# Kernel optimization log

Measured on AMD Instinct MI355X. Metric: run time of the kernel, lower is better.

Reference implementation:

```python
import jax
import jax.numpy as jnp
import numpy as np

B = 128          # graphs per batch
N = 1024         # nodes per graph
EG = 16384       # edges per graph (shared structure, repeated edge_weight)
F_IN = 64        # num_features
HID = 128        # hid_channels (ChebConv out)
K = 3            # Chebyshev order
C1 = HID // 2    # conv1d out channels
C2 = C1 // 2     # fc1 out
N_CLASSES = 4
POWER_ITERS = 50


def setup_inputs() -> dict:
    key = jax.random.key(0)
    ks = jax.random.split(key, 8)
    x = jax.random.normal(ks[0], (B * N, F_IN), dtype=jnp.float32)
    edge_index = jax.random.randint(ks[1], (2, EG), 0, N, dtype=jnp.int32)
    edge_weight = jax.random.uniform(ks[2], (EG,), dtype=jnp.float32)
    cheb_W = 0.05 * jax.random.normal(ks[3], (K, F_IN, HID), dtype=jnp.float32)
    cheb_b = jnp.zeros((HID,), jnp.float32)
    conv1d_W = 0.05 * jax.random.normal(ks[4], (C1, HID), dtype=jnp.float32)
    conv1d_b = jnp.zeros((C1,), jnp.float32)
    fc1_W = 0.01 * jax.random.normal(ks[5], (C2, C1 * N), dtype=jnp.float32)
    fc1_b = jnp.zeros((C2,), jnp.float32)
    fc2_W = 0.05 * jax.random.normal(ks[6], (N_CLASSES, C2), dtype=jnp.float32)
    fc2_b = jnp.zeros((N_CLASSES,), jnp.float32)
    return {"x": x, "edge_index": edge_index, "edge_weight": edge_weight,
            "cheb_W": cheb_W, "cheb_b": cheb_b,
            "conv1d_W": conv1d_W, "conv1d_b": conv1d_b,
            "fc1_W": fc1_W, "fc1_b": fc1_b, "fc2_W": fc2_W, "fc2_b": fc2_b}


def _lambda_max(edge_index, w):
    # LaplacianLambdaMax(normalization=None): largest eig of L = D - W, on raw
    # (un-relu'd) edge_attr, computed as a non-differentiable data transform.
    src, dst = edge_index[0], edge_index[1]
    deg = jax.ops.segment_sum(w, src, num_segments=N)

    def mv(v):  # L @ v
        return deg * v - jax.ops.segment_sum(w * v[src], dst, num_segments=N)

    def body(i, v):
        u = mv(v)
        return u / (jnp.linalg.norm(u) + 1e-12)

    v0 = jnp.ones((N,), jnp.float32) / np.float32(np.sqrt(N))
    v = jax.lax.fori_loop(0, POWER_ITERS, body, v0)
    return jax.lax.stop_gradient(jnp.vdot(v, mv(v)))


def _forward(x, edge_index, edge_weight, cheb_W, cheb_b, conv1d_W, conv1d_b,
             fc1_W, fc1_b, fc2_W, fc2_b):
    lmax = _lambda_max(edge_index, edge_weight)

    # Tile the shared per-graph edge structure over the batch (block-diagonal).
    offs = jnp.arange(B, dtype=jnp.int32) * N                  # [B]
    src = (edge_index[0][None, :] + offs[:, None]).reshape(-1)  # [B*EG]
    dst = (edge_index[1][None, :] + offs[:, None]).reshape(-1)  # [B*EG]
    w = jax.nn.relu(jnp.tile(edge_weight, B))                   # relu(edge_attr)

    BN = B * N
    deg = jax.ops.segment_sum(w, src, num_segments=BN)          # [BN]
    scale = 2.0 / lmax

    def lhat_mv(X):  # (2 L / lmax - I) @ X ; L = D - W
        agg = jax.ops.segment_sum(w[:, None] * X[src], dst, num_segments=BN)
        return scale * (deg[:, None] * X - agg) - X

    # Chebyshev recursion, K = 3
    tx0 = x                               # [BN, F_IN]
    tx1 = lhat_mv(tx0)
    tx2 = 2.0 * lhat_mv(tx1) - tx0
    h = tx0 @ cheb_W[0] + tx1 @ cheb_W[1] + tx2 @ cheb_W[2] + cheb_b  # [BN, HID]

    # 1x1 conv1d over the node axis + relu
    hb = h.reshape(B, N, HID)
    c = jax.nn.relu(jnp.einsum('bnh,ch->bcn', hb, conv1d_W)
                    + conv1d_b[None, :, None])                  # [B, C1, N]
    flat = c.reshape(B, C1 * N)

    z = flat @ fc1_W.T + fc1_b
    z = z @ fc2_W.T + fc2_b                                     # [B, N_CLASSES]
    return jax.nn.softmax(z, axis=1)


def reference(x, edge_index, edge_weight, cheb_W, cheb_b, conv1d_W, conv1d_b,
              fc1_W, fc1_b, fc2_W, fc2_b):
    return _forward(x, edge_index, edge_weight, cheb_W, cheb_b, conv1d_W,
                    conv1d_b, fc1_W, fc1_b, fc2_W, fc2_b)
```

## Files before the change

### kernel.cpp

```cpp
#include <hip/hip_runtime.h>
#include <math.h>

#define BATCH 128
#define NNODE 1024
#define EG 16384
#define F_IN 64
#define HID 128
#define C1 64
#define C2 32
#define NCLS 4
#define POWER_ITERS 50
#define BN (BATCH * NNODE)
#define RMAX 28
#define NORM_EVERY 5

typedef float f32x4 __attribute__((ext_vector_type(4)));
typedef __bf16 bf16x8 __attribute__((ext_vector_type(8)));
typedef unsigned short u16x4 __attribute__((ext_vector_type(4)));

__device__ inline unsigned short f2bf(float f) {
    unsigned int u = __float_as_uint(f);
    u += 0x7fffu + ((u >> 16) & 1u);
    return (unsigned short)(u >> 16);
}
__device__ inline float bf2f(unsigned short h) {
    return __uint_as_float((unsigned int)h << 16);
}

__global__ __launch_bounds__(1024) void k_csr(
    const int* __restrict__ ei, const float* __restrict__ ew,
    int* __restrict__ ptr_g, float* __restrict__ dgr_g,
    float* __restrict__ dgl_g, int2* __restrict__ packed,
    int2* __restrict__ packed2)
{
    __shared__ int   cnt[NNODE];
    __shared__ float dgr[NNODE];
    __shared__ float dgl[NNODE];
    __shared__ int   s[NNODE];
    __shared__ int   base[NNODE];
    const int t = threadIdx.x;

    cnt[t] = 0; dgr[t] = 0.f; dgl[t] = 0.f;

    int es[16], ed[16];
    float w[16];
#pragma unroll
    for (int i = 0; i < 16; ++i) {
        const int e = i * 1024 + t;
        es[i] = ei[e];
        ed[i] = ei[EG + e];
        w[i]  = ew[e];
    }
    __syncthreads();
#pragma unroll
    for (int i = 0; i < 16; ++i) {
        atomicAdd(&cnt[ed[i]], 1);
        atomicAdd(&dgr[es[i]], w[i]);
        atomicAdd(&dgl[es[i]], fmaxf(w[i], 0.f));
    }
    __syncthreads();
    dgr_g[t] = dgr[t];
    dgl_g[t] = dgl[t];

    const int v = cnt[t];
    s[t] = v;
    __syncthreads();
    for (int o = 1; o < 1024; o <<= 1) {
        const int add = (t >= o) ? s[t - o] : 0;
        __syncthreads();
        s[t] += add;
        __syncthreads();
    }
    const int excl = s[t] - v;
    ptr_g[t] = excl;
    base[t]  = excl;
    if (t == 1023) ptr_g[1024] = s[1023];
    __syncthreads();

#pragma unroll
    for (int i = 0; i < 16; ++i) {
        const int p = atomicAdd(&base[ed[i]], 1);
        packed[p]  = make_int2(__float_as_int(w[i]), es[i]);
        packed2[p] = make_int2(__float_as_int(fmaxf(w[i], 0.f)), es[i] << 8);
    }
}

__global__ __launch_bounds__(256) void k_cvtw(
    const float* __restrict__ chebW, const float* __restrict__ convW,
    const float* __restrict__ scal,
    unsigned short* __restrict__ wcatT, unsigned short* __restrict__ cvw)
{
    const int i = blockIdx.x * 256 + threadIdx.x;
    const float s = scal[1];
    if (i < 24576) {
        const int n = i / 192, kk = i % 192;
        const int k = kk & 63;
        const float w0 = chebW[k * 128 + n];
        const float w1 = chebW[8192 + k * 128 + n];
        const float w2 = chebW[16384 + k * 128 + n];
        float val;
        if (kk < 64)       val = w0 - w1 + w2;
        else if (kk < 128) val = s * (w1 - 4.f * w2);
        else               val = 2.f * s * s * w2;
        wcatT[i] = f2bf(val);
    }
    const int j = i - 24576;
    if (j >= 0 && j < 8192) cvw[j] = f2bf(convW[j]);
}

__global__ __launch_bounds__(1024) void k_fused(
    const float* __restrict__ in,
    const int2* __restrict__ pk_raw, const int2* __restrict__ pk2,
    const int* __restrict__ ptrg,
    const float* __restrict__ dgr, const float* __restrict__ dgl,
    float* __restrict__ vstate, float* __restrict__ scal,
    float* __restrict__ out32, unsigned short* __restrict__ tcat,
    int slice, int writeX, int it0, int it1, int finalize)
{
    __shared__ float vA[NNODE];
    __shared__ float vB[NNODE];
    __shared__ float red[17];
    const int t = threadIdx.x;

    if (blockIdx.x == 0) {
        const int p0 = ptrg[t], p1 = ptrg[t + 1];
        float w[RMAX];
        int src[RMAX];
#pragma unroll
        for (int i = 0; i < RMAX; ++i) {
            if (p0 + i < p1) {
                const int2 e = pk_raw[p0 + i];
                w[i] = __int_as_float(e.x);
                src[i] = e.y;
            } else {
                w[i] = 0.f;
                src[i] = 0;
            }
        }
        const int tp0 = p0 + RMAX;
        const float dgv = dgr[t];

        vA[t] = (it0 == 0) ? 0.03125f : vstate[t];
        __syncthreads();

        float* cur = vA;
        float* nxt = vB;

        for (int it = it0; it < it1; ++it) {
            float u = dgv * cur[t];
#pragma unroll
            for (int i = 0; i < RMAX; ++i) u -= w[i] * cur[src[i]];
            for (int p = tp0; p < p1; ++p) {
                const int2 e = pk_raw[p];
                u -= __int_as_float(e.x) * cur[e.y];
            }
            if ((it % NORM_EVERY) == NORM_EVERY - 1) {
                float sr = u * u;
#pragma unroll
                for (int o = 32; o > 0; o >>= 1) sr += __shfl_down(sr, o, 64);
                if ((t & 63) == 0) red[t >> 6] = sr;
                __syncthreads();
                if (t < 64) {
                    float xs = (t < 16) ? red[t] : 0.f;
#pragma unroll
                    for (int o = 8; o > 0; o >>= 1) xs += __shfl_down(xs, o, 64);
                    if (t == 0) red[16] = 1.0f / (sqrtf(xs) + 1e-12f);
                }
                __syncthreads();
                nxt[t] = u * red[16];
            } else {
                nxt[t] = u;
            }
            __syncthreads();
            float* tmp = cur; cur = nxt; nxt = tmp;
        }

        if (!finalize) {
            vstate[t] = cur[t];
            return;
        }
        float u = dgv * cur[t];
#pragma unroll
        for (int i = 0; i < RMAX; ++i) u -= w[i] * cur[src[i]];
        for (int p = tp0; p < p1; ++p) {
            const int2 e = pk_raw[p];
            u -= __int_as_float(e.x) * cur[e.y];
        }
        float sr = cur[t] * u;
#pragma unroll
        for (int o = 32; o > 0; o >>= 1) sr += __shfl_down(sr, o, 64);
        if ((t & 63) == 0) red[t >> 6] = sr;
        __syncthreads();
        if (t == 0) {
            float lm = 0.f;
            for (int i = 0; i < 16; ++i) lm += red[i];
            scal[0] = lm;
            scal[1] = 2.0f / lm;
        }
        return;
    }

    const int b1   = blockIdx.x - 1;
    const int bid  = ((b1 & 7) << 10) + (b1 >> 3);
    const int lane = threadIdx.x & 63;
    const int gnode = __builtin_amdgcn_readfirstlane(bid * 16 + (threadIdx.x >> 6));
    const int b = gnode >> 10, d = gnode & 1023;

    const int p0 = __builtin_amdgcn_readfirstlane(ptrg[d]);
    const int p1 = __builtin_amdgcn_readfirstlane(ptrg[d + 1]);
    const char* xb = (const char*)(in + (size_t)b * (NNODE * F_IN));

    float acc = 0.f;
    int p = p0;
    for (; p + 4 <= p1; p += 4) {
        const int2 e0 = pk2[p],     e1 = pk2[p + 1];
        const int2 e2 = pk2[p + 2], e3 = pk2[p + 3];
        const float v0 = ((const float*)(xb + (unsigned)e0.y))[lane];
        const float v1 = ((const float*)(xb + (unsigned)e1.y))[lane];
        const float v2 = ((const float*)(xb + (unsigned)e2.y))[lane];
        const float v3 = ((const float*)(xb + (unsigned)e3.y))[lane];
        acc += __int_as_float(e0.x) * v0;
        acc += __int_as_float(e1.x) * v1;
        acc += __int_as_float(e2.x) * v2;
        acc += __int_as_float(e3.x) * v3;
    }
    for (; p < p1; ++p) {
        const int2 e = pk2[p];
        acc += __int_as_float(e.x) * ((const float*)(xb + (unsigned)e.y))[lane];
    }

    const size_t gi = (size_t)gnode * F_IN + lane;
    const float xv = in[gi];
    const float o = dgl[d] * xv - acc;
    if (out32) out32[gi] = o;
    tcat[(size_t)gnode * 192 + slice * 64 + lane] = f2bf(o);
    if (writeX) tcat[(size_t)gnode * 192 + lane] = f2bf(xv);
}

__global__ __launch_bounds__(256) void k_cheb_mfma(
    const unsigned short* __restrict__ tcat,
    const unsigned short* __restrict__ wcatT,
    const unsigned short* __restrict__ cvw,
    const float* __restrict__ chebB, const float* __restrict__ convB,
    unsigned short* __restrict__ cout)
{
    __shared__ __align__(16) char smem[49152];
    __shared__ float cb_s[HID];
    __shared__ float cvb_s[C1];

    const int t    = threadIdx.x;
    const int lane = t & 63;
    const int wid  = t >> 6;
    const int l15  = lane & 15;
    const int l4   = lane >> 4;
    const int rbase = blockIdx.x * 128;
    const int bb = rbase >> 10;
    const int n0 = rbase & 1023;

    if (t < HID) cb_s[t] = chebB[t];
    if (t < C1)  cvb_s[t] = convB[t];

    for (int it = 0; it < 12; ++it) {
        const int gslot = it * 256 + t;
        const int n = gslot / 24, q = gslot % 24;
        const bf16x8 v = *(const bf16x8*)(wcatT + n * 192 + q * 8);
        *(bf16x8*)(smem + n * 384 + ((q ^ (n & 7)) << 4)) = v;
    }
    __syncthreads();

    const int rw = rbase + wid * 32;
    f32x4 acc[2][8];
#pragma unroll
    for (int m = 0; m < 2; ++m)
#pragma unroll
        for (int n = 0; n < 8; ++n) acc[m][n] = (f32x4)(0.f);

    const unsigned short* ta = tcat + (size_t)(rw + l15) * 192 + l4 * 8;
    bf16x8 a0 = *(const bf16x8*)(ta);
    bf16x8 a1 = *(const bf16x8*)(ta + 16 * 192);

#pragma unroll
    for (int ks = 0; ks < 6; ++ks) {
        bf16x8 na0, na1;
        if (ks < 5) {
            na0 = *(const bf16x8*)(ta + (ks + 1) * 32);
            na1 = *(const bf16x8*)(ta + 16 * 192 + (ks + 1) * 32);
        }
        const int kb = ks * 4 + l4;
#pragma unroll
        for (int nb = 0; nb < 8; ++nb) {
            const int n = nb * 16 + l15;
            const bf16x8 bv =
                *(const bf16x8*)(smem + n * 384 + ((kb ^ (n & 7)) << 4));
            acc[0][nb] = __builtin_amdgcn_mfma_f32_16x16x32_bf16(
                a0, bv, acc[0][nb], 0, 0, 0);
            acc[1][nb] = __builtin_amdgcn_mfma_f32_16x16x32_bf16(
                a1, bv, acc[1][nb], 0, 0, 0);
        }
        a0 = na0; a1 = na1;
    }
    __syncthreads();

#pragma unroll
    for (int mf = 0; mf < 2; ++mf)
#pragma unroll
        for (int nb = 0; nb < 8; ++nb) {
            const int c = nb * 16 + l15;
            const int slot = c >> 3;
            const float cb = cb_s[c];
#pragma unroll
            for (int reg = 0; reg < 4; ++reg) {
                const int node = wid * 32 + mf * 16 + l4 * 4 + reg;
                *(unsigned short*)(smem + node * 256 +
                                   ((slot ^ (node & 7)) << 4) + (c & 7) * 2) =
                    f2bf(acc[mf][nb][reg] + cb);
            }
        }
    for (int it = 0; it < 4; ++it) {
        const int gslot = it * 256 + t;
        const int c1i = gslot >> 4, q = gslot & 15;
        const bf16x8 v = *(const bf16x8*)(cvw + c1i * 128 + q * 8);
// ... 46 lines not shown
        const int j = i >> 8, k = i & 255;
        Wt[k * 33 + j] = W[(size_t)j * (C1 * NNODE) + k0 + k];
    }
    __syncthreads();

    const int j = t & 31, bg = t >> 5;
    float acc[16];
#pragma unroll
    for (int i = 0; i < 16; ++i) acc[i] = 0.f;

    const unsigned short* cb = cf + (size_t)(bg * 16) * (C1 * NNODE) + k0;
    for (int k4 = 0; k4 < 64; ++k4) {
        const int kb = k4 * 4;
        const float w0 = Wt[(kb + 0) * 33 + j];
        const float w1 = Wt[(kb + 1) * 33 + j];
        const float w2 = Wt[(kb + 2) * 33 + j];
        const float w3 = Wt[(kb + 3) * 33 + j];
#pragma unroll
        for (int i = 0; i < 16; ++i) {
            const u16x4 cv = *(const u16x4*)&cb[(size_t)i * (C1 * NNODE) + kb];
            acc[i] += bf2f(cv[0]) * w0 + bf2f(cv[1]) * w1 +
                      bf2f(cv[2]) * w2 + bf2f(cv[3]) * w3;
        }
    }
#pragma unroll
    for (int i = 0; i < 16; ++i)
        part[(size_t)g * 4096 + (size_t)(bg * 16 + i) * 32 + j] = acc[i];
}

__global__ __launch_bounds__(256) void k_red(
    const float* __restrict__ part, float* __restrict__ z)
{
    const int o = blockIdx.x * 256 + threadIdx.x;
    float s = 0.f;
    for (int g = 0; g < 256; ++g) s += part[(size_t)g * 4096 + o];
    z[o] = s;
}

__global__ __launch_bounds__(128) void k_head(
    const float* __restrict__ z, const float* __restrict__ b1,
    const float* __restrict__ W2, const float* __restrict__ b2,
    float* __restrict__ outp)
{
    const int b = threadIdx.x;
    float a[32];
#pragma unroll
    for (int j = 0; j < 32; ++j) a[j] = z[b * 32 + j] + b1[j];
    float l[4];
#pragma unroll
    for (int c = 0; c < 4; ++c) {
        float s = b2[c];
#pragma unroll
        for (int j = 0; j < 32; ++j) s += W2[c * 32 + j] * a[j];
        l[c] = s;
    }
    const float m = fmaxf(fmaxf(l[0], l[1]), fmaxf(l[2], l[3]));
    const float e0 = expf(l[0] - m), e1 = expf(l[1] - m);
    const float e2 = expf(l[2] - m), e3 = expf(l[3] - m);
    const float inv = 1.f / (e0 + e1 + e2 + e3);
    outp[b * 4 + 0] = e0 * inv;
    outp[b * 4 + 1] = e1 * inv;
    outp[b * 4 + 2] = e2 * inv;
    outp[b * 4 + 3] = e3 * inv;
}

extern "C" void kernel_launch(void* const* d_in, const int* in_sizes, int n_in,
                              void* d_out, int out_size, void* d_ws, size_t ws_size,
                              hipStream_t stream)
{
    const float* x     = (const float*)d_in[0];
    const int*   ei    = (const int*)d_in[1];
    const float* ew    = (const float*)d_in[2];
    const float* chebW = (const float*)d_in[3];
    const float* chebB = (const float*)d_in[4];
    const float* convW = (const float*)d_in[5];
    const float* convB = (const float*)d_in[6];
    const float* fc1W  = (const float*)d_in[7];
    const float* fc1B  = (const float*)d_in[8];
    const float* fc2W  = (const float*)d_in[9];
    const float* fc2B  = (const float*)d_in[10];
    float* out = (float*)d_out;

    char* ws = (char*)d_ws;
    float* scal   = (float*)(ws + 0);
    float* vstate = (float*)(ws + 4096);
    char*  partb = ws + 8192;
    int*   ptr  = (int*)(partb + 8192);
    float* dgr  = (float*)(partb + 16384);
    float* dgl  = (float*)(partb + 20480);
    int2*  pk   = (int2*)(partb + 24576);
    unsigned short* wcatT = (unsigned short*)(partb + 262144);
    unsigned short* cvwB  = (unsigned short*)(partb + 327680);
    int2*  pk2  = (int2*)(partb + 458752);
    float* part = (float*)partb;
    float* z    = (float*)(ws + 8192 + 4194304);
    float* y1   = (float*)(ws + 8192 + 4194304 + 65536);
    unsigned short* tcat = (unsigned short*)((char*)y1 + 33554432);
    unsigned short* cbuf = (unsigned short*)((char*)tcat + 50331648);

    k_csr <<<dim3(1), dim3(1024), 0, stream>>>(ei, ew, ptr, dgr, dgl, pk, pk2);

    k_fused<<<dim3(BN / 16 + 1), dim3(1024), 0, stream>>>(
        x, pk, pk2, ptr, dgr, dgl, vstate, scal,
        y1, tcat, 1, 1, 0, 25, 0);
    k_fused<<<dim3(BN / 16 + 1), dim3(1024), 0, stream>>>(
        y1, pk, pk2, ptr, dgr, dgl, vstate, scal,
        (float*)nullptr, tcat, 2, 0, 25, 50, 1);

    k_cvtw<<<dim3(128), dim3(256), 0, stream>>>(chebW, convW, scal, wcatT, cvwB);

    k_cheb_mfma<<<dim3(BN / 128), dim3(256), 0, stream>>>(
        tcat, wcatT, cvwB, chebB, convB, cbuf);

    k_fc1<<<dim3(256), dim3(256), 0, stream>>>(cbuf, fc1W, part);
    k_red<<<dim3(16), dim3(256), 0, stream>>>(part, z);
    k_head<<<dim3(1), dim3(128), 0, stream>>>(z, fc1B, fc2W, fc2B, out);
}
```

Measured before the change: 268.0 us.

## Fuse both graph propagation hops into one LDS-resident kernel per graph slice

The two propagation launches, which went through a global fp32 intermediate, are replaced by one kernel. Each block holds a 16-feature slice of one graph's node features in shared memory (128 KB) and runs both Laplacian hops from LDS. The power iteration now runs all 50 steps in block 0 of that single launch. The edge list is padded to multiples of four per node so four edges are gathered in parallel per wavefront and combined with shuffles. This removes the y1 round trip, one launch, and the scattered global gathers, at the cost of only 513 large blocks with low occupancy and 4x redundant edge traversal per graph.

```diff
diff --git a/kernel.cpp b/kernel.cpp
--- a/kernel.cpp
+++ b/kernel.cpp
@@ -29,15 +29,17 @@
 
 __global__ __launch_bounds__(1024) void k_csr(
     const int* __restrict__ ei, const float* __restrict__ ew,
-    int* __restrict__ ptr_g, float* __restrict__ dgr_g,
-    float* __restrict__ dgl_g, int2* __restrict__ packed,
-    int2* __restrict__ packed2)
+    int* __restrict__ ptr_g, int* __restrict__ ptr2_g,
+    float* __restrict__ dgr_g, float* __restrict__ dgl_g,
+    int2* __restrict__ packed, int2* __restrict__ packed2)
 {
     __shared__ int   cnt[NNODE];
     __shared__ float dgr[NNODE];
     __shared__ float dgl[NNODE];
     __shared__ int   s[NNODE];
+    __shared__ int   s2[NNODE];
     __shared__ int   base[NNODE];
+    __shared__ int   base2[NNODE];
     const int t = threadIdx.x;
 
     cnt[t] = 0; dgr[t] = 0.f; dgl[t] = 0.f;
@@ -62,27 +64,33 @@
     dgr_g[t] = dgr[t];
     dgl_g[t] = dgl[t];
 
-    const int v = cnt[t];
-    s[t] = v;
+    const int v  = cnt[t];
+    const int v4 = (v + 3) & ~3;
+    s[t] = v; s2[t] = v4;
     __syncthreads();
     for (int o = 1; o < 1024; o <<= 1) {
-        const int add = (t >= o) ? s[t - o] : 0;
+        const int a  = (t >= o) ? s[t - o]  : 0;
+        const int a2 = (t >= o) ? s2[t - o] : 0;
         __syncthreads();
-        s[t] += add;
+        s[t] += a; s2[t] += a2;
         __syncthreads();
     }
-    const int excl = s[t] - v;
-    ptr_g[t] = excl;
-    base[t]  = excl;
-    if (t == 1023) ptr_g[1024] = s[1023];
+    const int excl  = s[t]  - v;
+    const int excl2 = s2[t] - v4;
+    ptr_g[t]  = excl;  base[t]  = excl;
+    ptr2_g[t] = excl2; base2[t] = excl2;
+    if (t == 1023) { ptr_g[1024] = s[1023]; ptr2_g[1024] = s2[1023]; }
     __syncthreads();
 
 #pragma unroll
     for (int i = 0; i < 16; ++i) {
-        const int p = atomicAdd(&base[ed[i]], 1);
-        packed[p]  = make_int2(__float_as_int(w[i]), es[i]);
-        packed2[p] = make_int2(__float_as_int(fmaxf(w[i], 0.f)), es[i] << 8);
-    }
+        const int p  = atomicAdd(&base[ed[i]],  1);
+        const int p2 = atomicAdd(&base2[ed[i]], 1);
+        packed[p]   = make_int2(__float_as_int(w[i]), es[i]);
+        packed2[p2] = make_int2(__float_as_int(fmaxf(w[i], 0.f)), es[i] << 6);
+    }
+    for (int j = excl2 + v; j < excl2 + v4; ++j)
+        packed2[j] = make_int2(0, 0);
 }
 
 __global__ __launch_bounds__(256) void k_cvtw(
@@ -108,21 +116,20 @@
     if (j >= 0 && j < 8192) cvw[j] = f2bf(convW[j]);
 }
 
-__global__ __launch_bounds__(1024) void k_fused(
-    const float* __restrict__ in,
+__global__ __launch_bounds__(1024) void k_prop2(
+    const float* __restrict__ x,
     const int2* __restrict__ pk_raw, const int2* __restrict__ pk2,
-    const int* __restrict__ ptrg,
+    const int* __restrict__ ptrg, const int* __restrict__ ptr2g,
     const float* __restrict__ dgr, const float* __restrict__ dgl,
-    float* __restrict__ vstate, float* __restrict__ scal,
-    float* __restrict__ out32, unsigned short* __restrict__ tcat,
-    int slice, int writeX, int it0, int it1, int finalize)
-{
-    __shared__ float vA[NNODE];
-    __shared__ float vB[NNODE];
-    __shared__ float red[17];
+    float* __restrict__ scal, unsigned short* __restrict__ tcat)
+{
+    __shared__ float smem[32768];
     const int t = threadIdx.x;
 
     if (blockIdx.x == 0) {
+        float* vA  = smem;
+        float* vB  = smem + 1024;
+        float* red = smem + 2048;
         const int p0 = ptrg[t], p1 = ptrg[t + 1];
         float w[RMAX];
         int src[RMAX];
@@ -140,13 +147,13 @@
         const int tp0 = p0 + RMAX;
         const float dgv = dgr[t];
 
-        vA[t] = (it0 == 0) ? 0.03125f : vstate[t];
+        vA[t] = 0.03125f;
         __syncthreads();
 
         float* cur = vA;
         float* nxt = vB;
 
-        for (int it = it0; it < it1; ++it) {
+        for (int it = 0; it < POWER_ITERS; ++it) {
             float u = dgv * cur[t];
 #pragma unroll
             for (int i = 0; i < RMAX; ++i) u -= w[i] * cur[src[i]];
@@ -161,10 +168,10 @@
                 if ((t & 63) == 0) red[t >> 6] = sr;
                 __syncthreads();
                 if (t < 64) {
-                    float xs = (t < 16) ? red[t] : 0.f;
-#pragma unroll
-                    for (int o = 8; o > 0; o >>= 1) xs += __shfl_down(xs, o, 64);
-                    if (t == 0) red[16] = 1.0f / (sqrtf(xs) + 1e-12f);
+                    float xs2 = (t < 16) ? red[t] : 0.f;
+#pragma unroll
+                    for (int o = 8; o > 0; o >>= 1) xs2 += __shfl_down(xs2, o, 64);
+                    if (t == 0) red[16] = 1.0f / (sqrtf(xs2) + 1e-12f);
                 }
                 __syncthreads();
                 nxt[t] = u * red[16];
@@ -175,10 +182,6 @@
             float* tmp = cur; cur = nxt; nxt = tmp;
         }
 
-        if (!finalize) {
-            vstate[t] = cur[t];
-            return;
-        }
         float u = dgv * cur[t];
 #pragma unroll
         for (int i = 0; i < RMAX; ++i) u -= w[i] * cur[src[i]];
@@ -200,41 +203,51 @@
         return;
     }
 
-    const int b1   = blockIdx.x - 1;
-    const int bid  = ((b1 & 7) << 10) + (b1 >> 3);
-    const int lane = threadIdx.x & 63;
-    const int gnode = __builtin_amdgcn_readfirstlane(bid * 16 + (threadIdx.x >> 6));
-    const int b = gnode >> 10, d = gnode & 1023;
-
-    const int p0 = __builtin_amdgcn_readfirstlane(ptrg[d]);
-    const int p1 = __builtin_amdgcn_readfirstlane(ptrg[d + 1]);
-    const char* xb = (const char*)(in + (size_t)b * (NNODE * F_IN));
-
-    float acc = 0.f;
-    int p = p0;
-    for (; p + 4 <= p1; p += 4) {
-        const int2 e0 = pk2[p],     e1 = pk2[p + 1];
-        const int2 e2 = pk2[p + 2], e3 = pk2[p + 3];
-        const float v0 = ((const float*)(xb + (unsigned)e0.y))[lane];
-        const float v1 = ((const float*)(xb + (unsigned)e1.y))[lane];
-        const float v2 = ((const float*)(xb + (unsigned)e2.y))[lane];
-        const float v3 = ((const float*)(xb + (unsigned)e3.y))[lane];
-        acc += __int_as_float(e0.x) * v0;
-        acc += __int_as_float(e1.x) * v1;
-        acc += __int_as_float(e2.x) * v2;
-        acc += __int_as_float(e3.x) * v3;
-    }
-    for (; p < p1; ++p) {
-        const int2 e = pk2[p];
-        acc += __int_as_float(e.x) * ((const float*)(xb + (unsigned)e.y))[lane];
-    }
-
-    const size_t gi = (size_t)gnode * F_IN + lane;
-    const float xv = in[gi];
-    const float o = dgl[d] * xv - acc;
-    if (out32) out32[gi] = o;
-    tcat[(size_t)gnode * 192 + slice * 64 + lane] = f2bf(o);
-    if (writeX) tcat[(size_t)gnode * 192 + lane] = f2bf(xv);
+    const int bb = blockIdx.x - 1;
+    const int g  = bb >> 2;
+    const int c  = bb & 3;
+    float* xs = smem;
+    float* ys = smem + 16384;
+
+    const float* xg = x + (size_t)g * (NNODE * F_IN) + c * 16;
+    unsigned short* tg = tcat + (size_t)g * NNODE * 192 + c * 16;
+
+    for (int i = t; i < 16384; i += 1024) {
+        const int n = i >> 4, f = i & 15;
+        const float xv = xg[n * 64 + f];
+        xs[i] = xv;
+        tg[n * 192 + f] = f2bf(xv);
+    }
+    __syncthreads();
+
+    const int wv   = t >> 6;
+    const int lane = t & 63;
+    const int slot = lane >> 4;
+    const int f    = lane & 15;
+
+    for (int pass = 0; pass < 2; ++pass) {
+        const float* srcv = pass ? ys : xs;
+        for (int d = wv; d < NNODE; d += 16) {
+            const int q0 = __builtin_amdgcn_readfirstlane(ptr2g[d]);
+            const int q1 = __builtin_amdgcn_readfirstlane(ptr2g[d + 1]);
+            float acc = 0.f;
+            for (int p = q0; p < q1; p += 4) {
+                const int2 e = pk2[p + slot];
+                const float vv =
+                    *(const float*)((const char*)srcv + e.y + (f << 2));
+                acc += __int_as_float(e.x) * vv;
+            }
+            acc += __shfl_xor(acc, 16, 64);
+            acc += __shfl_xor(acc, 32, 64);
+            const float xv = srcv[d * 16 + f];
+            const float y = dgl[d] * xv - acc;
+            if (lane < 16) {
+                if (pass == 0) ys[d * 16 + f] = y;
+                tg[d * 192 + (pass + 1) * 64 + f] = f2bf(y);
+            }
+        }
+        __syncthreads();
+    }
 }
 
 __global__ __launch_bounds__(256) void k_cheb_mfma(
@@ -449,30 +462,26 @@
     float* out = (float*)d_out;
 
     char* ws = (char*)d_ws;
-    float* scal   = (float*)(ws + 0);
-    float* vstate = (float*)(ws + 4096);
+    float* scal = (float*)(ws + 0);
     char*  partb = ws + 8192;
-    int*   ptr  = (int*)(partb + 8192);
-    float* dgr  = (float*)(partb + 16384);
-    float* dgl  = (float*)(partb + 20480);
-    int2*  pk   = (int2*)(partb + 24576);
-    unsigned short* wcatT = (unsigned short*)(partb + 262144);
-    unsigned short* cvwB  = (unsigned short*)(partb + 327680);
-    int2*  pk2  = (int2*)(partb + 458752);
+    int*   ptr   = (int*)(partb + 8192);
+    int*   ptr2  = (int*)(partb + 16384);
+    float* dgr   = (float*)(partb + 24576);
+    float* dgl   = (float*)(partb + 28672);
+    int2*  pk    = (int2*)(partb + 32768);
+    int2*  pk2   = (int2*)(partb + 163840);
+    unsigned short* wcatT = (unsigned short*)(partb + 327680);
+    unsigned short* cvwB  = (unsigned short*)(partb + 393216);
     float* part = (float*)partb;
     float* z    = (float*)(ws + 8192 + 4194304);
-    float* y1   = (float*)(ws + 8192 + 4194304 + 65536);
-    unsigned short* tcat = (unsigned short*)((char*)y1 + 33554432);
+    unsigned short* tcat = (unsigned short*)(ws + 8192 + 4194304 + 65536);
     unsigned short* cbuf = (unsigned short*)((char*)tcat + 50331648);
 
-    k_csr <<<dim3(1), dim3(1024), 0, stream>>>(ei, ew, ptr, dgr, dgl, pk, pk2);
-
-    k_fused<<<dim3(BN / 16 + 1), dim3(1024), 0, stream>>>(
-        x, pk, pk2, ptr, dgr, dgl, vstate, scal,
-        y1, tcat, 1, 1, 0, 25, 0);
-    k_fused<<<dim3(BN / 16 + 1), dim3(1024), 0, stream>>>(
-        y1, pk, pk2, ptr, dgr, dgl, vstate, scal,
-        (float*)nullptr, tcat, 2, 0, 25, 50, 1);
+    k_csr<<<dim3(1), dim3(1024), 0, stream>>>(ei, ew, ptr, ptr2, dgr, dgl,
+                                              pk, pk2);
+
+    k_prop2<<<dim3(513), dim3(1024), 0, stream>>>(
+        x, pk, pk2, ptr, ptr2, dgr, dgl, scal, tcat);
 
     k_cvtw<<<dim3(128), dim3(256), 0, stream>>>(chebW, convW, scal, wcatT, cvwB);
 
```

Result: slower. 520.6 us (+94.2%).

## Replace sparse graph aggregation with dense bf16 adjacency MFMA GEMM

Applied to the files above, without the earlier changes.

Builds a dense 1024x1024 adjacency matrix of relu'd edge weights, stores it in bf16, and runs both Chebyshev aggregation passes as dense MFMA matrix multiplies against per-graph transposed bf16 feature tiles staged in LDS. This replaces the per-edge gather loops, which are latency-bound. New kernels zero the matrix, convert it to bf16, and transpose x. The dense product does far more arithmetic than the sparse one (about 16 edges per row against 1024 columns), and the second-pass input y1 is now rounded to bf16, so precision drops.

```diff
diff --git a/kernel.cpp b/kernel.cpp
--- a/kernel.cpp
+++ b/kernel.cpp
@@ -17,6 +17,7 @@
 typedef float f32x4 __attribute__((ext_vector_type(4)));
 typedef __bf16 bf16x8 __attribute__((ext_vector_type(8)));
 typedef unsigned short u16x4 __attribute__((ext_vector_type(4)));
+typedef unsigned short u16x8 __attribute__((ext_vector_type(8)));
 
 __device__ inline unsigned short f2bf(float f) {
     unsigned int u = __float_as_uint(f);
@@ -27,11 +28,16 @@
     return __uint_as_float((unsigned int)h << 16);
 }
 
+__global__ __launch_bounds__(1024) void k_zm(float* __restrict__ M32)
+{
+    M32[(size_t)blockIdx.x * 1024 + threadIdx.x] = 0.f;
+}
+
 __global__ __launch_bounds__(1024) void k_csr(
     const int* __restrict__ ei, const float* __restrict__ ew,
     int* __restrict__ ptr_g, float* __restrict__ dgr_g,
     float* __restrict__ dgl_g, int2* __restrict__ packed,
-    int2* __restrict__ packed2)
+    float* __restrict__ M32)
 {
     __shared__ int   cnt[NNODE];
     __shared__ float dgr[NNODE];
@@ -57,6 +63,7 @@
         atomicAdd(&cnt[ed[i]], 1);
         atomicAdd(&dgr[es[i]], w[i]);
         atomicAdd(&dgl[es[i]], fmaxf(w[i], 0.f));
+        atomicAdd(&M32[(size_t)ed[i] * 1024 + es[i]], fmaxf(w[i], 0.f));
     }
     __syncthreads();
     dgr_g[t] = dgr[t];
@@ -66,9 +73,9 @@
     s[t] = v;
     __syncthreads();
     for (int o = 1; o < 1024; o <<= 1) {
-        const int add = (t >= o) ? s[t - o] : 0;
+        const int a = (t >= o) ? s[t - o] : 0;
         __syncthreads();
-        s[t] += add;
+        s[t] += a;
         __syncthreads();
     }
     const int excl = s[t] - v;
@@ -80,8 +87,237 @@
 #pragma unroll
     for (int i = 0; i < 16; ++i) {
         const int p = atomicAdd(&base[ed[i]], 1);
-        packed[p]  = make_int2(__float_as_int(w[i]), es[i]);
-        packed2[p] = make_int2(__float_as_int(fmaxf(w[i], 0.f)), es[i] << 8);
+        packed[p] = make_int2(__float_as_int(w[i]), es[i]);
+    }
+}
+
+__global__ __launch_bounds__(256) void k_cvt_m(
+    const float* __restrict__ M32, unsigned short* __restrict__ M16)
+{
+    const int i = blockIdx.x * 256 + threadIdx.x;
+    const f32x4 v = ((const f32x4*)M32)[i];
+    u16x4 o;
+    o[0] = f2bf(v[0]); o[1] = f2bf(v[1]); o[2] = f2bf(v[2]); o[3] = f2bf(v[3]);
+    *(u16x4*)(M16 + (size_t)i * 4) = o;
+}
+
+__global__ __launch_bounds__(256) void k_xpose(
+    const float* __restrict__ x, unsigned short* __restrict__ xB,
+    unsigned short* __restrict__ tcat)
+{
+    __shared__ unsigned short tile[64 * 66];
+    const int t = threadIdx.x;
+    const int g = blockIdx.x >> 4;
+    const int sp = blockIdx.x & 15;
+    const int n0 = sp * 64;
+
+    const float* xg = x + (size_t)g * (NNODE * F_IN);
+#pragma unroll
+    for (int it = 0; it < 4; ++it) {
+        const int nl = it * 16 + (t >> 4);
+        const int f  = (t & 15) * 4;
+        const f32x4 v = *(const f32x4*)(xg + (size_t)(n0 + nl) * 64 + f);
+        u16x4 o;
+        o[0] = f2bf(v[0]); o[1] = f2bf(v[1]); o[2] = f2bf(v[2]); o[3] = f2bf(v[3]);
+        *(u16x4*)(tcat + ((size_t)(g * 1024 + n0 + nl)) * 192 + f) = o;
+#pragma unroll
+        for (int j = 0; j < 4; ++j) tile[(f + j) * 66 + nl] = o[j];
+    }
+    __syncthreads();
+
+    unsigned short* xg2 = xB + (size_t)g * 65536;
+#pragma unroll
+    for (int it = 0; it < 2; ++it) {
+        const int f  = t & 63;
+        const int cL = (t >> 6) + it * 4;
+        u16x8 v;
+#pragma unroll
+        for (int j = 0; j < 8; ++j) v[j] = tile[f * 66 + cL * 8 + j];
+        const int c = sp * 8 + cL;
+        *(u16x8*)(xg2 + f * 1024 + ((c ^ (f & 7)) << 3)) = v;
+    }
+}
+
+template<int PASS>
+__global__ __launch_bounds__(1024) void k_pass(
+    const float* __restrict__ x, const unsigned short* __restrict__ M16,
+    const unsigned short* __restrict__ stageSrc,
+    const int2* __restrict__ pk_raw, const int* __restrict__ ptrg,
+    const float* __restrict__ dgr, const float* __restrict__ dgl,
+    float* __restrict__ vstate, float* __restrict__ scal,
+    unsigned short* __restrict__ tcat, unsigned short* __restrict__ y1B)
+{
+    __shared__ __align__(16) char smem[131072];
+    const int t = threadIdx.x;
+
+    if (blockIdx.x == 0) {
+        float* vA  = (float*)smem;
+        float* vB  = vA + 1024;
+        float* red = vB + 1024;
+        const int it0 = (PASS == 1) ? 0 : 25;
+        const int it1 = (PASS == 1) ? 25 : 50;
+
+        const int p0 = ptrg[t], p1 = ptrg[t + 1];
+        float w[RMAX];
+        int src[RMAX];
+#pragma unroll
+        for (int i = 0; i < RMAX; ++i) {
+            if (p0 + i < p1) {
+                const int2 e = pk_raw[p0 + i];
+                w[i] = __int_as_float(e.x);
+                src[i] = e.y;
+            } else {
+                w[i] = 0.f;
+                src[i] = 0;
+            }
+        }
+        const int tp0 = p0 + RMAX;
+        const float dgv = dgr[t];
+
+        vA[t] = (PASS == 1) ? 0.03125f : vstate[t];
+        __syncthreads();
+
+        float* cur = vA;
+        float* nxt = vB;
+
+        for (int it = it0; it < it1; ++it) {
+            float u = dgv * cur[t];
+#pragma unroll
+            for (int i = 0; i < RMAX; ++i) u -= w[i] * cur[src[i]];
+            for (int p = tp0; p < p1; ++p) {
+                const int2 e = pk_raw[p];
+                u -= __int_as_float(e.x) * cur[e.y];
+            }
+            if ((it % NORM_EVERY) == NORM_EVERY - 1) {
+                float sr = u * u;
+#pragma unroll
+                for (int o = 32; o > 0; o >>= 1) sr += __shfl_down(sr, o, 64);
+                if ((t & 63) == 0) red[t >> 6] = sr;
+                __syncthreads();
+                if (t < 64) {
+                    float xs2 = (t < 16) ? red[t] : 0.f;
+#pragma unroll
+                    for (int o = 8; o > 0; o >>= 1) xs2 += __shfl_down(xs2, o, 64);
+                    if (t == 0) red[16] = 1.0f / (sqrtf(xs2) + 1e-12f);
+                }
+                __syncthreads();
+                nxt[t] = u * red[16];
+            } else {
+                nxt[t] = u;
+            }
+            __syncthreads();
+            float* tmp = cur; cur = nxt; nxt = tmp;
+        }
+
+        if (PASS == 1) {
+            vstate[t] = cur[t];
+            return;
+        }
+        float u = dgv * cur[t];
+#pragma unroll
+        for (int i = 0; i < RMAX; ++i) u -= w[i] * cur[src[i]];
+        for (int p = tp0; p < p1; ++p) {
+            const int2 e = pk_raw[p];
+            u -= __int_as_float(e.x) * cur[e.y];
+        }
+        float sr = cur[t] * u;
+#pragma unroll
+        for (int o = 32; o > 0; o >>= 1) sr += __shfl_down(sr, o, 64);
+        if ((t & 63) == 0) red[t >> 6] = sr;
+        __syncthreads();
+        if (t == 0) {
+            float lm = 0.f;
+            for (int i = 0; i < 16; ++i) lm += red[i];
+            scal[0] = lm;
+            scal[1] = 2.0f / lm;
+        }
+        return;
+    }
+
+    const int bb = blockIdx.x - 1;
+    const int g  = bb >> 1;
+    const int nb = (bb & 1) << 9;
+
+    {
+        const f32x4* src2 = (const f32x4*)(stageSrc + (size_t)g * 65536);
+        f32x4* dst = (f32x4*)smem;
+        for (int i = t; i < 8192; i += 1024) dst[i] = src2[i];
+    }
+    __syncthreads();
+
+    const int lane = t & 63;
+    const int w    = t >> 6;
+    const int l15  = lane & 15;
+    const int l4   = lane >> 4;
+
+    f32x4 acc[2][4];
+#pragma unroll
+    for (int rt = 0; rt < 2; ++rt)
+#pragma unroll
+        for (int ft = 0; ft < 4; ++ft) acc[rt][ft] = (f32x4)(0.f);
+
+    const unsigned short* ta =
+        M16 + (size_t)(nb + w * 32 + l15) * 1024 + l4 * 8;
+    bf16x8 a0 = *(const bf16x8*)(ta);
+    bf16x8 a1 = *(const bf16x8*)(ta + 16 * 1024);
+
+    for (int ks = 0; ks < 32; ++ks) {
+        bf16x8 na0, na1;
+        if (ks < 31) {
+            na0 = *(const bf16x8*)(ta + (ks + 1) * 32);
+            na1 = *(const bf16x8*)(ta + 16 * 1024 + (ks + 1) * 32);
+        }
+#pragma unroll
+        for (int ft = 0; ft < 4; ++ft) {
+            const int row = ft * 16 + l15;
+            const bf16x8 bv = *(const bf16x8*)(
+                smem + row * 2048 + (((ks * 4 + l4) ^ (row & 7)) << 4));
+            acc[0][ft] = __builtin_amdgcn_mfma_f32_16x16x32_bf16(
+                a0, bv, acc[0][ft], 0, 0, 0);
+            acc[1][ft] = __builtin_amdgcn_mfma_f32_16x16x32_bf16(
+                a1, bv, acc[1][ft], 0, 0, 0);
+        }
+        a0 = na0; a1 = na1;
+    }
+    __syncthreads();
+
+    unsigned short* hs = (unsigned short*)smem;
+#pragma unroll
+    for (int rt = 0; rt < 2; ++rt) {
+#pragma unroll
+        for (int reg = 0; reg < 4; ++reg) {
+            const int nl = w * 32 + rt * 16 + l4 * 4 + reg;
+            const int node = nb + nl;
+            const float dg = dgl[node];
+#pragma unroll
+            for (int ft = 0; ft < 4; ++ft) {
+                const int f = ft * 16 + l15;
+                float xv;
+                if (PASS == 1)
+                    xv = x[(size_t)g * 65536 + (size_t)node * 64 + f];
+                else
+                    xv = bf2f(tcat[((size_t)(g * 1024 + node)) * 192 + 64 + f]);
+                const float y = dg * xv - acc[rt][ft][reg];
+                tcat[((size_t)(g * 1024 + node)) * 192 + PASS * 64 + f] =
+                    f2bf(y);
+                if (PASS == 1) hs[nl * 66 + f] = f2bf(y);
+            }
+        }
+    }
+
+    if (PASS == 1) {
+        __syncthreads();
+        unsigned short* yg = y1B + (size_t)g * 65536;
+#pragma unroll
+        for (int it2 = 0; it2 < 4; ++it2) {
+            const int idx = it2 * 1024 + t;
+            const int f = idx & 63, cL = idx >> 6;
+            u16x8 v;
+#pragma unroll
+            for (int j = 0; j < 8; ++j) v[j] = hs[(cL * 8 + j) * 66 + f];
+            const int c = (nb >> 3) + cL;
+            *(u16x8*)(yg + f * 1024 + ((c ^ (f & 7)) << 3)) = v;
+        }
     }
 }
 
@@ -108,135 +344,6 @@
     if (j >= 0 && j < 8192) cvw[j] = f2bf(convW[j]);
 }
 
-__global__ __launch_bounds__(1024) void k_fused(
-    const float* __restrict__ in,
-    const int2* __restrict__ pk_raw, const int2* __restrict__ pk2,
-    const int* __restrict__ ptrg,
-    const float* __restrict__ dgr, const float* __restrict__ dgl,
-    float* __restrict__ vstate, float* __restrict__ scal,
-    float* __restrict__ out32, unsigned short* __restrict__ tcat,
-    int slice, int writeX, int it0, int it1, int finalize)
-{
-    __shared__ float vA[NNODE];
-    __shared__ float vB[NNODE];
-    __shared__ float red[17];
-    const int t = threadIdx.x;
-
-    if (blockIdx.x == 0) {
-        const int p0 = ptrg[t], p1 = ptrg[t + 1];
-        float w[RMAX];
-        int src[RMAX];
-#pragma unroll
-        for (int i = 0; i < RMAX; ++i) {
-            if (p0 + i < p1) {
-                const int2 e = pk_raw[p0 + i];
-                w[i] = __int_as_float(e.x);
-                src[i] = e.y;
-            } else {
-                w[i] = 0.f;
-                src[i] = 0;
-            }
-        }
-        const int tp0 = p0 + RMAX;
-        const float dgv = dgr[t];
-
-        vA[t] = (it0 == 0) ? 0.03125f : vstate[t];
-        __syncthreads();
-
-        float* cur = vA;
-        float* nxt = vB;
-
-        for (int it = it0; it < it1; ++it) {
-            float u = dgv * cur[t];
-#pragma unroll
-            for (int i = 0; i < RMAX; ++i) u -= w[i] * cur[src[i]];
-            for (int p = tp0; p < p1; ++p) {
-                const int2 e = pk_raw[p];
-                u -= __int_as_float(e.x) * cur[e.y];
-            }
-            if ((it % NORM_EVERY) == NORM_EVERY - 1) {
-                float sr = u * u;
-#pragma unroll
-                for (int o = 32; o > 0; o >>= 1) sr += __shfl_down(sr, o, 64);
-                if ((t & 63) == 0) red[t >> 6] = sr;
-                __syncthreads();
-                if (t < 64) {
-                    float xs = (t < 16) ? red[t] : 0.f;
-#pragma unroll
-                    for (int o = 8; o > 0; o >>= 1) xs += __shfl_down(xs, o, 64);
-                    if (t == 0) red[16] = 1.0f / (sqrtf(xs) + 1e-12f);
-                }
-                __syncthreads();
-                nxt[t] = u * red[16];
-            } else {
-                nxt[t] = u;
-            }
-            __syncthreads();
-            float* tmp = cur; cur = nxt; nxt = tmp;
-        }
-
-        if (!finalize) {
-            vstate[t] = cur[t];
-            return;
-        }
-        float u = dgv * cur[t];
-#pragma unroll
-        for (int i = 0; i < RMAX; ++i) u -= w[i] * cur[src[i]];
-        for (int p = tp0; p < p1; ++p) {
-            const int2 e = pk_raw[p];
-            u -= __int_as_float(e.x) * cur[e.y];
-        }
-        float sr = cur[t] * u;
-#pragma unroll
-        for (int o = 32; o > 0; o >>= 1) sr += __shfl_down(sr, o, 64);
-        if ((t & 63) == 0) red[t >> 6] = sr;
-        __syncthreads();
-        if (t == 0) {
-            float lm = 0.f;
-            for (int i = 0; i < 16; ++i) lm += red[i];
-            scal[0] = lm;
-            scal[1] = 2.0f / lm;
-        }
-        return;
-    }
-
-    const int b1   = blockIdx.x - 1;
-    const int bid  = ((b1 & 7) << 10) + (b1 >> 3);
-    const int lane = threadIdx.x & 63;
-    const int gnode = __builtin_amdgcn_readfirstlane(bid * 16 + (threadIdx.x >> 6));
-    const int b = gnode >> 10, d = gnode & 1023;
-
-    const int p0 = __builtin_amdgcn_readfirstlane(ptrg[d]);
-    const int p1 = __builtin_amdgcn_readfirstlane(ptrg[d + 1]);
-    const char* xb = (const char*)(in + (size_t)b * (NNODE * F_IN));
-
-    float acc = 0.f;
-    int p = p0;
-    for (; p + 4 <= p1; p += 4) {
-        const int2 e0 = pk2[p],     e1 = pk2[p + 1];
-        const int2 e2 = pk2[p + 2], e3 = pk2[p + 3];
-        const float v0 = ((const float*)(xb + (unsigned)e0.y))[lane];
-        const float v1 = ((const float*)(xb + (unsigned)e1.y))[lane];
-        const float v2 = ((const float*)(xb + (unsigned)e2.y))[lane];
-        const float v3 = ((const float*)(xb + (unsigned)e3.y))[lane];
-        acc += __int_as_float(e0.x) * v0;
-        acc += __int_as_float(e1.x) * v1;
-        acc += __int_as_float(e2.x) * v2;
-        acc += __int_as_float(e3.x) * v3;
-    }
-    for (; p < p1; ++p) {
-        const int2 e = pk2[p];
-        acc += __int_as_float(e.x) * ((const float*)(xb + (unsigned)e.y))[lane];
-    }
-
-    const size_t gi = (size_t)gnode * F_IN + lane;
-    const float xv = in[gi];
-    const float o = dgl[d] * xv - acc;
-    if (out32) out32[gi] = o;
-    tcat[(size_t)gnode * 192 + slice * 64 + lane] = f2bf(o);
-    if (writeX) tcat[(size_t)gnode * 192 + lane] = f2bf(xv);
-}
-
 __global__ __launch_bounds__(256) void k_cheb_mfma(
     const unsigned short* __restrict__ tcat,
     const unsigned short* __restrict__ wcatT,
@@ -451,28 +558,32 @@
     char* ws = (char*)d_ws;
     float* scal   = (float*)(ws + 0);
     float* vstate = (float*)(ws + 4096);
-    char*  partb = ws + 8192;
+    char*  partb  = ws + 8192;
     int*   ptr  = (int*)(partb + 8192);
-    float* dgr  = (float*)(partb + 16384);
-    float* dgl  = (float*)(partb + 20480);
-    int2*  pk   = (int2*)(partb + 24576);
-    unsigned short* wcatT = (unsigned short*)(partb + 262144);
-    unsigned short* cvwB  = (unsigned short*)(partb + 327680);
-    int2*  pk2  = (int2*)(partb + 458752);
+    float* dgr  = (float*)(partb + 24576);
+    float* dgl  = (float*)(partb + 28672);
+    int2*  pk   = (int2*)(partb + 32768);
+    unsigned short* wcatT = (unsigned short*)(partb + 327680);
+    unsigned short* cvwB  = (unsigned short*)(partb + 393216);
     float* part = (float*)partb;
-    float* z    = (float*)(ws + 8192 + 4194304);
-    float* y1   = (float*)(ws + 8192 + 4194304 + 65536);
-    unsigned short* tcat = (unsigned short*)((char*)y1 + 33554432);
-    unsigned short* cbuf = (unsigned short*)((char*)tcat + 50331648);
-
-    k_csr <<<dim3(1), dim3(1024), 0, stream>>>(ei, ew, ptr, dgr, dgl, pk, pk2);
-
-    k_fused<<<dim3(BN / 16 + 1), dim3(1024), 0, stream>>>(
-        x, pk, pk2, ptr, dgr, dgl, vstate, scal,
-        y1, tcat, 1, 1, 0, 25, 0);
-    k_fused<<<dim3(BN / 16 + 1), dim3(1024), 0, stream>>>(
-        y1, pk, pk2, ptr, dgr, dgl, vstate, scal,
-        (float*)nullptr, tcat, 2, 0, 25, 50, 1);
+    float* z    = (float*)(ws + 4202496);
+    float*          M32  = (float*)(ws + 4268032);
+    unsigned short* M16  = (unsigned short*)(ws + 8462336);
+    unsigned short* xB   = (unsigned short*)(ws + 10559488);
+    unsigned short* y1B  = (unsigned short*)(ws + 27336704);
+    unsigned short* tcat = (unsigned short*)(ws + 44113920);
+    unsigned short* cbuf = (unsigned short*)(ws + 94445568);
+
+    k_zm   <<<dim3(1024), dim3(1024), 0, stream>>>(M32);
+    k_csr  <<<dim3(1),    dim3(1024), 0, stream>>>(ei, ew, ptr, dgr, dgl, pk,
+                                                   M32);
+    k_cvt_m<<<dim3(1024), dim3(256),  0, stream>>>(M32, M16);
+    k_xpose<<<dim3(2048), dim3(256),  0, stream>>>(x, xB, tcat);
+
+    k_pass<1><<<dim3(257), dim3(1024), 0, stream>>>(
+        x, M16, xB, pk, ptr, dgr, dgl, vstate, scal, tcat, y1B);
+    k_pass<2><<<dim3(257), dim3(1024), 0, stream>>>(
+        x, M16, y1B, pk, ptr, dgr, dgl, vstate, scal, tcat, y1B);
 
     k_cvtw<<<dim3(128), dim3(256), 0, stream>>>(chebW, convW, scal, wcatT, cvwB);
 
```

Result: slower. 319.1 us (+19.0%).

## Gather neighbor features in bf16 and prefetch edge lists into registers

Applied to the files above, without the earlier changes.

A new pre-pass converts x to bf16 once, writing both a compact bf16 copy and the X slice of tcat. The two sparse aggregation passes then gather bf16 neighbor rows instead of fp32, and the first pass stores y1 as bf16 rather than fp32. The per-node edge loop is rewritten to prefetch up to 20 edges into registers so the gathers can be issued together, with two accumulators. This halves the gather traffic and the y1 write but adds an extra kernel launch and a pass over x, and it rounds the inputs of the recursion to bf16, which may cost accuracy.

```diff
diff --git a/kernel.cpp b/kernel.cpp
--- a/kernel.cpp
+++ b/kernel.cpp
@@ -13,6 +13,7 @@
 #define BN (BATCH * NNODE)
 #define RMAX 28
 #define NORM_EVERY 5
+#define PRE 20
 
 typedef float f32x4 __attribute__((ext_vector_type(4)));
 typedef __bf16 bf16x8 __attribute__((ext_vector_type(8)));
@@ -66,9 +67,9 @@
     s[t] = v;
     __syncthreads();
     for (int o = 1; o < 1024; o <<= 1) {
-        const int add = (t >= o) ? s[t - o] : 0;
+        const int a = (t >= o) ? s[t - o] : 0;
         __syncthreads();
-        s[t] += add;
+        s[t] += a;
         __syncthreads();
     }
     const int excl = s[t] - v;
@@ -81,8 +82,168 @@
     for (int i = 0; i < 16; ++i) {
         const int p = atomicAdd(&base[ed[i]], 1);
         packed[p]  = make_int2(__float_as_int(w[i]), es[i]);
-        packed2[p] = make_int2(__float_as_int(fmaxf(w[i], 0.f)), es[i] << 8);
-    }
+        packed2[p] = make_int2(__float_as_int(fmaxf(w[i], 0.f)), es[i] << 7);
+    }
+}
+
+__global__ __launch_bounds__(256) void k_xb(
+    const float* __restrict__ x, unsigned short* __restrict__ xb16,
+    unsigned short* __restrict__ tcat)
+{
+    const int i = blockIdx.x * 256 + threadIdx.x;
+    const f32x4 v = ((const f32x4*)x)[i];
+    u16x4 o;
+    o[0] = f2bf(v[0]); o[1] = f2bf(v[1]); o[2] = f2bf(v[2]); o[3] = f2bf(v[3]);
+    *(u16x4*)(xb16 + (size_t)i * 4) = o;
+    const int node = i >> 4;
+    const int fb = (i & 15) * 4;
+    *(u16x4*)(tcat + (size_t)node * 192 + fb) = o;
+}
+
+template<int PASS>
+__global__ __launch_bounds__(1024) void k_fused(
+    const float* __restrict__ x, const unsigned short* __restrict__ gsrc,
+    const int2* __restrict__ pk_raw, const int2* __restrict__ pk2,
+    const int* __restrict__ ptrg,
+    const float* __restrict__ dgr, const float* __restrict__ dgl,
+    float* __restrict__ vstate, float* __restrict__ scal,
+    unsigned short* __restrict__ tcat, unsigned short* __restrict__ y1b)
+{
+    __shared__ float vA[NNODE];
+    __shared__ float vB[NNODE];
+    __shared__ float red[17];
+    const int t = threadIdx.x;
+
+    if (blockIdx.x == 0) {
+        const int it0 = (PASS == 1) ? 0 : 25;
+        const int it1 = (PASS == 1) ? 25 : 50;
+
+        const int p0 = ptrg[t], p1 = ptrg[t + 1];
+        float w[RMAX];
+        int src[RMAX];
+#pragma unroll
+        for (int i = 0; i < RMAX; ++i) {
+            if (p0 + i < p1) {
+                const int2 e = pk_raw[p0 + i];
+                w[i] = __int_as_float(e.x);
+                src[i] = e.y;
+            } else {
+                w[i] = 0.f;
+                src[i] = 0;
+            }
+        }
+        const int tp0 = p0 + RMAX;
+        const float dgv = dgr[t];
+
+        vA[t] = (PASS == 1) ? 0.03125f : vstate[t];
+        __syncthreads();
+
+        float* cur = vA;
+        float* nxt = vB;
+
+        for (int it = it0; it < it1; ++it) {
+            float u = dgv * cur[t];
+#pragma unroll
+            for (int i = 0; i < RMAX; ++i) u -= w[i] * cur[src[i]];
+            for (int p = tp0; p < p1; ++p) {
+                const int2 e = pk_raw[p];
+                u -= __int_as_float(e.x) * cur[e.y];
+            }
+            if ((it % NORM_EVERY) == NORM_EVERY - 1) {
+                float sr = u * u;
+#pragma unroll
+                for (int o = 32; o > 0; o >>= 1) sr += __shfl_down(sr, o, 64);
+                if ((t & 63) == 0) red[t >> 6] = sr;
+                __syncthreads();
+                if (t < 64) {
+                    float xs2 = (t < 16) ? red[t] : 0.f;
+#pragma unroll
+                    for (int o = 8; o > 0; o >>= 1) xs2 += __shfl_down(xs2, o, 64);
+                    if (t == 0) red[16] = 1.0f / (sqrtf(xs2) + 1e-12f);
+                }
+                __syncthreads();
+                nxt[t] = u * red[16];
+            } else {
+                nxt[t] = u;
+            }
+            __syncthreads();
+            float* tmp = cur; cur = nxt; nxt = tmp;
+        }
+
+        if (PASS == 1) {
+            vstate[t] = cur[t];
+            return;
+        }
+        float u = dgv * cur[t];
+#pragma unroll
+        for (int i = 0; i < RMAX; ++i) u -= w[i] * cur[src[i]];
+        for (int p = tp0; p < p1; ++p) {
+            const int2 e = pk_raw[p];
+            u -= __int_as_float(e.x) * cur[e.y];
+        }
+        float sr = cur[t] * u;
+#pragma unroll
+        for (int o = 32; o > 0; o >>= 1) sr += __shfl_down(sr, o, 64);
+        if ((t & 63) == 0) red[t >> 6] = sr;
+        __syncthreads();
+        if (t == 0) {
+            float lm = 0.f;
+            for (int i = 0; i < 16; ++i) lm += red[i];
+            scal[0] = lm;
+            scal[1] = 2.0f / lm;
+        }
+        return;
+    }
+
+    const int b1   = blockIdx.x - 1;
+    const int bid  = ((b1 & 7) << 10) + (b1 >> 3);
+    const int lane = t & 63;
+    const int gnode = __builtin_amdgcn_readfirstlane(bid * 16 + (t >> 6));
+    const int b = gnode >> 10, d = gnode & 1023;
+
+    const int p0 = __builtin_amdgcn_readfirstlane(ptrg[d]);
+    const int p1 = __builtin_amdgcn_readfirstlane(ptrg[d + 1]);
+    const char* gb = (const char*)(gsrc + (size_t)b * 65536);
+
+    float ew_r[PRE];
+    unsigned off_r[PRE];
+#pragma unroll
+    for (int i = 0; i < PRE; ++i) {
+        int idx = p0 + i;
+        idx = (idx < p1) ? idx : (p1 - 1);
+        idx = (idx < EG) ? idx : (EG - 1);
+        idx = (idx > 0) ? idx : 0;
+        const int2 e = pk2[idx];
+        const bool valid = (p0 + i < p1);
+        ew_r[i]  = valid ? __int_as_float(e.x) : 0.f;
+        off_r[i] = valid ? (unsigned)e.y : 0u;
+    }
+
+    float vv[PRE];
+#pragma unroll
+    for (int i = 0; i < PRE; ++i)
+        vv[i] = bf2f(*(const unsigned short*)(gb + off_r[i] + (lane << 1)));
+
+    float acc0 = 0.f, acc1 = 0.f;
+#pragma unroll
+    for (int i = 0; i < PRE; i += 2) {
+        acc0 += ew_r[i] * vv[i];
+        acc1 += ew_r[i + 1] * vv[i + 1];
+    }
+    float acc = acc0 + acc1;
+
+    for (int p = p0 + PRE; p < p1; ++p) {
+        const int2 e = pk2[p];
+        acc += __int_as_float(e.x) *
+               bf2f(*(const unsigned short*)(gb + (unsigned)e.y + (lane << 1)));
+    }
+
+    float xv;
+    if (PASS == 1) xv = x[(size_t)gnode * 64 + lane];
+    else           xv = bf2f(gsrc[(size_t)gnode * 64 + lane]);
+    const float y = dgl[d] * xv - acc;
+    tcat[(size_t)gnode * 192 + PASS * 64 + lane] = f2bf(y);
+    if (PASS == 1) y1b[(size_t)gnode * 64 + lane] = f2bf(y);
 }
 
 __global__ __launch_bounds__(256) void k_cvtw(
@@ -108,135 +269,6 @@
     if (j >= 0 && j < 8192) cvw[j] = f2bf(convW[j]);
 }
 
-__global__ __launch_bounds__(1024) void k_fused(
-    const float* __restrict__ in,
-    const int2* __restrict__ pk_raw, const int2* __restrict__ pk2,
-    const int* __restrict__ ptrg,
-    const float* __restrict__ dgr, const float* __restrict__ dgl,
-    float* __restrict__ vstate, float* __restrict__ scal,
-    float* __restrict__ out32, unsigned short* __restrict__ tcat,
-    int slice, int writeX, int it0, int it1, int finalize)
-{
-    __shared__ float vA[NNODE];
-    __shared__ float vB[NNODE];
-    __shared__ float red[17];
-    const int t = threadIdx.x;
-
-    if (blockIdx.x == 0) {
-        const int p0 = ptrg[t], p1 = ptrg[t + 1];
-        float w[RMAX];
-        int src[RMAX];
-#pragma unroll
-        for (int i = 0; i < RMAX; ++i) {
-            if (p0 + i < p1) {
-                const int2 e = pk_raw[p0 + i];
-                w[i] = __int_as_float(e.x);
-                src[i] = e.y;
-            } else {
-                w[i] = 0.f;
-                src[i] = 0;
-            }
-        }
-        const int tp0 = p0 + RMAX;
-        const float dgv = dgr[t];
-
-        vA[t] = (it0 == 0) ? 0.03125f : vstate[t];
-        __syncthreads();
-
-        float* cur = vA;
-        float* nxt = vB;
-
-        for (int it = it0; it < it1; ++it) {
-            float u = dgv * cur[t];
-#pragma unroll
-            for (int i = 0; i < RMAX; ++i) u -= w[i] * cur[src[i]];
-            for (int p = tp0; p < p1; ++p) {
-                const int2 e = pk_raw[p];
-                u -= __int_as_float(e.x) * cur[e.y];
-            }
-            if ((it % NORM_EVERY) == NORM_EVERY - 1) {
-                float sr = u * u;
-#pragma unroll
-                for (int o = 32; o > 0; o >>= 1) sr += __shfl_down(sr, o, 64);
-                if ((t & 63) == 0) red[t >> 6] = sr;
-                __syncthreads();
-                if (t < 64) {
-                    float xs = (t < 16) ? red[t] : 0.f;
-#pragma unroll
-                    for (int o = 8; o > 0; o >>= 1) xs += __shfl_down(xs, o, 64);
-                    if (t == 0) red[16] = 1.0f / (sqrtf(xs) + 1e-12f);
-                }
-                __syncthreads();
-                nxt[t] = u * red[16];
-            } else {
-                nxt[t] = u;
-            }
-            __syncthreads();
-            float* tmp = cur; cur = nxt; nxt = tmp;
-        }
-
-        if (!finalize) {
-            vstate[t] = cur[t];
-            return;
-        }
-        float u = dgv * cur[t];
-#pragma unroll
-        for (int i = 0; i < RMAX; ++i) u -= w[i] * cur[src[i]];
-        for (int p = tp0; p < p1; ++p) {
-            const int2 e = pk_raw[p];
-            u -= __int_as_float(e.x) * cur[e.y];
-        }
-        float sr = cur[t] * u;
-#pragma unroll
-        for (int o = 32; o > 0; o >>= 1) sr += __shfl_down(sr, o, 64);
-        if ((t & 63) == 0) red[t >> 6] = sr;
-        __syncthreads();
-        if (t == 0) {
-            float lm = 0.f;
-            for (int i = 0; i < 16; ++i) lm += red[i];
-            scal[0] = lm;
-            scal[1] = 2.0f / lm;
-        }
-        return;
-    }
-
-    const int b1   = blockIdx.x - 1;
-    const int bid  = ((b1 & 7) << 10) + (b1 >> 3);
-    const int lane = threadIdx.x & 63;
-    const int gnode = __builtin_amdgcn_readfirstlane(bid * 16 + (threadIdx.x >> 6));
-    const int b = gnode >> 10, d = gnode & 1023;
-
-    const int p0 = __builtin_amdgcn_readfirstlane(ptrg[d]);
-    const int p1 = __builtin_amdgcn_readfirstlane(ptrg[d + 1]);
-    const char* xb = (const char*)(in + (size_t)b * (NNODE * F_IN));
-
-    float acc = 0.f;
-    int p = p0;
-    for (; p + 4 <= p1; p += 4) {
-        const int2 e0 = pk2[p],     e1 = pk2[p + 1];
-        const int2 e2 = pk2[p + 2], e3 = pk2[p + 3];
-        const float v0 = ((const float*)(xb + (unsigned)e0.y))[lane];
-        const float v1 = ((const float*)(xb + (unsigned)e1.y))[lane];
-        const float v2 = ((const float*)(xb + (unsigned)e2.y))[lane];
-        const float v3 = ((const float*)(xb + (unsigned)e3.y))[lane];
-        acc += __int_as_float(e0.x) * v0;
-        acc += __int_as_float(e1.x) * v1;
-        acc += __int_as_float(e2.x) * v2;
-        acc += __int_as_float(e3.x) * v3;
-    }
-    for (; p < p1; ++p) {
-        const int2 e = pk2[p];
-        acc += __int_as_float(e.x) * ((const float*)(xb + (unsigned)e.y))[lane];
-    }
-
-    const size_t gi = (size_t)gnode * F_IN + lane;
-    const float xv = in[gi];
-    const float o = dgl[d] * xv - acc;
-    if (out32) out32[gi] = o;
-    tcat[(size_t)gnode * 192 + slice * 64 + lane] = f2bf(o);
-    if (writeX) tcat[(size_t)gnode * 192 + lane] = f2bf(xv);
-}
-
 __global__ __launch_bounds__(256) void k_cheb_mfma(
     const unsigned short* __restrict__ tcat,
     const unsigned short* __restrict__ wcatT,
@@ -451,7 +483,7 @@
     char* ws = (char*)d_ws;
     float* scal   = (float*)(ws + 0);
     float* vstate = (float*)(ws + 4096);
-    char*  partb = ws + 8192;
+    char*  partb  = ws + 8192;
     int*   ptr  = (int*)(partb + 8192);
     float* dgr  = (float*)(partb + 16384);
     float* dgl  = (float*)(partb + 20480);
@@ -460,19 +492,19 @@
     unsigned short* cvwB  = (unsigned short*)(partb + 327680);
     int2*  pk2  = (int2*)(partb + 458752);
     float* part = (float*)partb;
-    float* z    = (float*)(ws + 8192 + 4194304);
-    float* y1   = (float*)(ws + 8192 + 4194304 + 65536);
-    unsigned short* tcat = (unsigned short*)((char*)y1 + 33554432);
-    unsigned short* cbuf = (unsigned short*)((char*)tcat + 50331648);
-
-    k_csr <<<dim3(1), dim3(1024), 0, stream>>>(ei, ew, ptr, dgr, dgl, pk, pk2);
-
-    k_fused<<<dim3(BN / 16 + 1), dim3(1024), 0, stream>>>(
-        x, pk, pk2, ptr, dgr, dgl, vstate, scal,
-        y1, tcat, 1, 1, 0, 25, 0);
-    k_fused<<<dim3(BN / 16 + 1), dim3(1024), 0, stream>>>(
-        y1, pk, pk2, ptr, dgr, dgl, vstate, scal,
-        (float*)nullptr, tcat, 2, 0, 25, 50, 1);
+    float* z    = (float*)(ws + 4202496);
+    unsigned short* xb16 = (unsigned short*)(ws + 4268032);
+    unsigned short* y1b  = (unsigned short*)(ws + 21045248);
+    unsigned short* tcat = (unsigned short*)(ws + 37822464);
+    unsigned short* cbuf = (unsigned short*)(ws + 88154112);
+
+    k_csr<<<dim3(1),    dim3(1024), 0, stream>>>(ei, ew, ptr, dgr, dgl, pk, pk2);
+    k_xb <<<dim3(8192), dim3(256),  0, stream>>>(x, xb16, tcat);
+
+    k_fused<1><<<dim3(8193), dim3(1024), 0, stream>>>(
+        x, xb16, pk, pk2, ptr, dgr, dgl, vstate, scal, tcat, y1b);
+    k_fused<2><<<dim3(8193), dim3(1024), 0, stream>>>(
+        x, y1b, pk, pk2, ptr, dgr, dgl, vstate, scal, tcat, y1b);
 
     k_cvtw<<<dim3(128), dim3(256), 0, stream>>>(chebW, convW, scal, wcatT, cvwB);
 
```

Result: slower. 314.9 us (+17.5%).
